# Kernel tuning notes

Measured on AMD Instinct MI355X. Metric: run time of the kernel, lower is better.

## Reference

```python
import jax, jax.numpy as jnp
import numpy as np

DIM = 512
NUM_HEADS = 8
HEAD_DIM = DIM // NUM_HEADS
B, S = 2, 2048


def setup_inputs() -> dict:
    key = jax.random.key(0)
    ks = jax.random.split(key, 16)
    scale = 1.0 / np.sqrt(DIM)
    inp = {
        "x": jax.random.normal(ks[0], (B, S, DIM), dtype=jnp.float32),
        "Qexpl": jax.random.normal(ks[1], (B, S, DIM), dtype=jnp.float32),
        "Kexpl": jax.random.normal(ks[2], (B, S, DIM), dtype=jnp.float32),
        "fl": jax.random.uniform(ks[3], (B,), dtype=jnp.float32),
        "fu": jax.random.uniform(ks[4], (B,), dtype=jnp.float32),
        "age": jax.random.uniform(ks[5], (B,), dtype=jnp.float32),
        "gender": jax.random.uniform(ks[6], (B,), dtype=jnp.float32),
        # Linear params: weight stored as [out, in] like torch; y = x @ W.T + b
        "Wq": jax.random.normal(ks[7], (DIM, DIM), dtype=jnp.float32) * scale,
        "bq": jnp.zeros((DIM,), dtype=jnp.float32),
        "Wk": jax.random.normal(ks[8], (DIM, DIM), dtype=jnp.float32) * scale,
        "bk": jnp.zeros((DIM,), dtype=jnp.float32),
        "Wv": jax.random.normal(ks[9], (DIM, DIM), dtype=jnp.float32) * scale,
        "bv": jnp.zeros((DIM,), dtype=jnp.float32),
        "Wo": jax.random.normal(ks[10], (DIM, DIM), dtype=jnp.float32) * scale,
        "bo": jnp.zeros((DIM,), dtype=jnp.float32),
    }
    return inp


def reference(x, Qexpl, Kexpl, fl, fu, age, gender, Wq, bq, Wk, bk, Wv, bv, Wo, bo):
    # drofe_fn is None -> Q/K projections used directly.
    Q = Qexpl @ Wq.T + bq            # [B, S, D]
    K = Kexpl @ Wk.T + bk            # [B, S, D]
    V = x @ Wv.T + bv                # [B, S, D]

    def split_heads(t):  # [B, S, D] -> [B, H, S, hd]
        return t.reshape(B, S, NUM_HEADS, HEAD_DIM).transpose(0, 2, 1, 3)

    Qh, Kh, Vh = split_heads(Q), split_heads(K), split_heads(V)
    scale = 1.0 / np.sqrt(HEAD_DIM).astype(np.float32)
    scores = jnp.einsum("bhqd,bhkd->bhqk", Qh, Kh) * scale  # [B, H, S, S]
    weights = jax.nn.softmax(scores, axis=-1)
    attn = jnp.einsum("bhqk,bhkd->bhqd", weights, Vh)        # [B, H, S, hd]
    attn = attn.transpose(0, 2, 1, 3).reshape(B, S, DIM)
    return attn @ Wo.T + bo
```

## Files before the change

kernel.cpp:

```cpp
#include <hip/hip_runtime.h>
#include <hip/hip_bf16.h>

typedef unsigned short ushort_t;
typedef __attribute__((ext_vector_type(8))) short bf16x8;
typedef __attribute__((ext_vector_type(4))) float f32x4;

__device__ __forceinline__ ushort_t f2bf(float f) {
    union { float f; unsigned u; } v; v.f = f;
    unsigned r = v.u + 0x7FFF + ((v.u >> 16) & 1);
    return (ushort_t)(r >> 16);
}
__device__ __forceinline__ bf16x8 ld8(const ushort_t* p) { return *(const bf16x8*)p; }

__device__ __forceinline__ unsigned cvt2(float x, float y) {
    __hip_bfloat162 h = __float22bfloat162_rn(make_float2(x, y));
    unsigned r; __builtin_memcpy(&r, &h, 4); return r;
}
__device__ __forceinline__ bf16x8 pack8(const float* p) {
    float4 a = *(const float4*)p;
    float4 b = *(const float4*)(p + 4);
    union { unsigned u[4]; bf16x8 v; } o;
    o.u[0] = cvt2(a.x, a.y); o.u[1] = cvt2(a.z, a.w);
    o.u[2] = cvt2(b.x, b.y); o.u[3] = cvt2(b.z, b.w);
    return o.v;
}

template <bool A_BF16, int OUT_MODE>
__device__ __forceinline__ void gemm_bt_tile(
    const void* __restrict__ Ap, const float* __restrict__ W,
    const float* __restrict__ bias, void* __restrict__ dstp,
    ushort_t* lA, ushort_t* lB, int m0, int n0)
{
    const ushort_t* Ab = (const ushort_t*)Ap;
    const float*    Af = (const float*)Ap;
    const int t = threadIdx.x;
    const int lane = t & 63;
    const int wave = t >> 6;
    const int wm = (wave & 1) * 64, wn = (wave >> 1) * 64;
    const int fr = lane & 15, quad = lane >> 4;

    f32x4 acc[4][4] = {};

    for (int k0 = 0; k0 < 512; k0 += 32) {
        bf16x8 va[2], vb[2];
#pragma unroll
        for (int i = 0; i < 2; ++i) {
            int s = i * 256 + t;
            int r = s >> 2, jp = s & 3;
            if (A_BF16)
                va[i] = ld8(Ab + (size_t)(m0 + r) * 512 + k0 + jp * 8);
            else
                va[i] = pack8(Af + (size_t)(m0 + r) * 512 + k0 + jp * 8);
            vb[i] = pack8(W + (size_t)(n0 + r) * 512 + k0 + jp * 8);
        }
        if (k0) __syncthreads();
#pragma unroll
        for (int i = 0; i < 2; ++i) {
            int s = i * 256 + t;
            int r = s >> 2, jp = s & 3;
            *(bf16x8*)(lA + r * 40 + jp * 8) = va[i];
            *(bf16x8*)(lB + r * 40 + jp * 8) = vb[i];
        }
        __syncthreads();

        bf16x8 af[4], bfrag[4];
#pragma unroll
        for (int mt = 0; mt < 4; ++mt)
            af[mt] = ld8(lA + (wm + mt * 16 + fr) * 40 + quad * 8);
#pragma unroll
        for (int nt = 0; nt < 4; ++nt)
            bfrag[nt] = ld8(lB + (wn + nt * 16 + fr) * 40 + quad * 8);
#pragma unroll
        for (int mt = 0; mt < 4; ++mt)
#pragma unroll
            for (int nt = 0; nt < 4; ++nt)
                acc[mt][nt] = __builtin_amdgcn_mfma_f32_16x16x32_bf16(
                    af[mt], bfrag[nt], acc[mt][nt], 0, 0, 0);
    }

#pragma unroll
    for (int nt = 0; nt < 4; ++nt) {
        int n = n0 + wn + nt * 16 + fr;
        float bb = bias[n];
#pragma unroll
        for (int mt = 0; mt < 4; ++mt) {
            int mb = m0 + wm + mt * 16 + quad * 4;
            if (OUT_MODE == 0) {
#pragma unroll
                for (int r = 0; r < 4; ++r)
                    ((ushort_t*)dstp)[(size_t)(mb + r) * 512 + n] = f2bf(acc[mt][nt][r] + bb);
            } else if (OUT_MODE == 1) {
#pragma unroll
                for (int r = 0; r < 4; ++r)
                    ((float*)dstp)[(size_t)(mb + r) * 512 + n] = acc[mt][nt][r] + bb;
            } else {
                int h = n >> 6, d = n & 63;
                int bidx = mb >> 11, s = mb & 2047;
                ushort4 pk;
                pk.x = f2bf(acc[mt][nt][0] + bb);
                pk.y = f2bf(acc[mt][nt][1] + bb);
                pk.z = f2bf(acc[mt][nt][2] + bb);
                pk.w = f2bf(acc[mt][nt][3] + bb);
                *(ushort4*)((ushort_t*)dstp + ((size_t)((bidx * 8 + h) * 64 + d)) * 2048 + s) = pk;
            }
        }
    }
}

__global__ __launch_bounds__(256, 2)
void proj_qkv_kernel(const float* __restrict__ Qe, const float* __restrict__ Ke,
                     const float* __restrict__ x,
                     const float* __restrict__ Wq, const float* __restrict__ bq,
                     const float* __restrict__ Wk, const float* __restrict__ bk,
                     const float* __restrict__ Wv, const float* __restrict__ bv,
                     ushort_t* __restrict__ Qo, ushort_t* __restrict__ Ko,
                     ushort_t* __restrict__ Vt)
{
    __shared__ ushort_t lA[128 * 40];
    __shared__ ushort_t lB[128 * 40];
    const int z = blockIdx.z;
    const float* A = (z == 0) ? Qe : (z == 1) ? Ke : x;
    const float* W = (z == 0) ? Wq : (z == 1) ? Wk : Wv;
    const float* bias = (z == 0) ? bq : (z == 1) ? bk : bv;
    ushort_t* dst = (z == 0) ? Qo : (z == 1) ? Ko : Vt;
    if (z == 2)
        gemm_bt_tile<false, 2>(A, W, bias, dst, lA, lB, blockIdx.y * 128, blockIdx.x * 128);
    else
        gemm_bt_tile<false, 0>(A, W, bias, dst, lA, lB, blockIdx.y * 128, blockIdx.x * 128);
}

__global__ __launch_bounds__(256, 2)
void gemm_o_kernel(const ushort_t* __restrict__ A, const float* __restrict__ W,
                   const float* __restrict__ bias, float* __restrict__ dst)
{
    __shared__ ushort_t lA[128 * 40];
    __shared__ ushort_t lB[128 * 40];
    gemm_bt_tile<true, 1>(A, W, bias, dst, lA, lB, blockIdx.y * 128, blockIdx.x * 128);
}

__global__ __launch_bounds__(256, 2)
void attn_kernel(const ushort_t* __restrict__ Q, const ushort_t* __restrict__ K,
                 const ushort_t* __restrict__ Vt, ushort_t* __restrict__ O)
{
    __shared__ ushort_t lQ[64 * 72];
    __shared__ ushort_t lK[128 * 72];
    __shared__ ushort_t lVt[64 * 136];
    __shared__ ushort_t lP[64 * 136];

    const int b = blockIdx.z, h = blockIdx.y;
    const int q0 = blockIdx.x * 64;
    const int t = threadIdx.x;
    const int lane = t & 63, wave = t >> 6;
    const int wq = wave * 16;
    const int fr = lane & 15, quad = lane >> 4;

#pragma unroll
    for (int i = 0; i < 2; ++i) {
        int s = i * 256 + t;
        int r = s >> 3, jp = s & 7;
        *(bf16x8*)(lQ + r * 72 + jp * 8) =
            ld8(Q + (size_t)(b * 2048 + q0 + r) * 512 + h * 64 + jp * 8);
    }

    const float C1 = 0.125f * 1.44269504088896340736f;
    const float FM = 12.0f;

    f32x4 oacc[4] = {};
    float lpart[4] = {};

    for (int kv = 0; kv < 2048; kv += 128) {
        bf16x8 vk[4], vv[4];
#pragma unroll
        for (int i = 0; i < 4; ++i) {
            int s = i * 256 + t;
            int r = s >> 3, jp = s & 7;
            vk[i] = ld8(K + (size_t)(b * 2048 + kv + r) * 512 + h * 64 + jp * 8);
            int r2 = s >> 4, jp2 = s & 15;
            vv[i] = ld8(Vt + (size_t)((b * 8 + h) * 64 + r2) * 2048 + kv + jp2 * 8);
        }
        __syncthreads();
#pragma unroll
        for (int i = 0; i < 4; ++i) {
            int s = i * 256 + t;
            int r = s >> 3, jp = s & 7;
            *(bf16x8*)(lK + r * 72 + jp * 8) = vk[i];
            int r2 = s >> 4, jp2 = s & 15;
            *(bf16x8*)(lVt + r2 * 136 + jp2 * 8) = vv[i];
        }
        __syncthreads();

        f32x4 sc[8] = {};
#pragma unroll
        for (int ks = 0; ks < 2; ++ks) {
            bf16x8 aq = ld8(lQ + (wq + fr) * 72 + (ks * 4 + quad) * 8);
#pragma unroll
            for (int nt = 0; nt < 8; ++nt) {
                bf16x8 kb = ld8(lK + (nt * 16 + fr) * 72 + (ks * 4 + quad) * 8);
                sc[nt] = __builtin_amdgcn_mfma_f32_16x16x32_bf16(aq, kb, sc[nt], 0, 0, 0);
            }
        }

#pragma unroll
        for (int r = 0; r < 4; ++r) {
            int row = wq + quad * 4 + r;
            float acc = 0.f;
#pragma unroll
            for (int nt = 0; nt < 8; ++nt) {
                float p = exp2f(sc[nt][r] * C1 - FM);
                acc += p;
                lP[row * 136 + nt * 16 + fr] = f2bf(p);
            }
            lpart[r] += acc;
        }

#pragma unroll
        for (int ks = 0; ks < 4; ++ks) {
            bf16x8 ap = ld8(lP + (wq + fr) * 136 + ks * 32 + quad * 8);
#pragma unroll
            for (int nt = 0; nt < 4; ++nt) {
                bf16x8 vb = ld8(lVt + (nt * 16 + fr) * 136 + ks * 32 + quad * 8);
                oacc[nt] = __builtin_amdgcn_mfma_f32_16x16x32_bf16(ap, vb, oacc[nt], 0, 0, 0);
            }
        }
    }

#pragma unroll
    for (int r = 0; r < 4; ++r) {
        float rs = lpart[r];
#pragma unroll
        for (int o = 1; o < 16; o <<= 1)
            rs += __shfl_xor(rs, o, 64);
        float inv = 1.f / rs;
        int q = q0 + wq + quad * 4 + r;
#pragma unroll
        for (int nt = 0; nt < 4; ++nt) {
            int d = nt * 16 + fr;
            O[(size_t)(b * 2048 + q) * 512 + h * 64 + d] = f2bf(oacc[nt][r] * inv);
        }
    }
}

extern "C" void kernel_launch(void* const* d_in, const int* in_sizes, int n_in,
                              void* d_out, int out_size, void* d_ws, size_t ws_size,
                              hipStream_t stream) {
    const float* x   = (const float*)d_in[0];
    const float* Qe  = (const float*)d_in[1];
    const float* Ke  = (const float*)d_in[2];
    const float* Wq  = (const float*)d_in[7];
    const float* bq  = (const float*)d_in[8];
    const float* Wk  = (const float*)d_in[9];
    const float* bk  = (const float*)d_in[10];
    const float* Wv  = (const float*)d_in[11];
    const float* bv  = (const float*)d_in[12];
    const float* Wo  = (const float*)d_in[13];
    const float* bo  = (const float*)d_in[14];

    const size_t NTOK = 2 * 2048;
    ushort_t* Qws = (ushort_t*)d_ws;
    ushort_t* Kws = Qws + NTOK * 512;
    ushort_t* Vt  = Kws + NTOK * 512;
    ushort_t* Ows = Vt  + NTOK * 512;

    proj_qkv_kernel<<<dim3(4, 32, 3), 256, 0, stream>>>(Qe, Ke, x, Wq, bq, Wk, bk, Wv, bv,
                                                        Qws, Kws, Vt);
    attn_kernel<<<dim3(32, 8, 2), 256, 0, stream>>>(Qws, Kws, Vt, Ows);
    gemm_o_kernel<<<dim3(4, 32, 1), 256, 0, stream>>>(Ows, Wo, bo, (float*)d_out);
}
```

Before: 182.8 us.

## Pre-convert inputs to bf16 and stage GEMM tiles via global_load_lds

Adds a conversion kernel that turns the fp32 activations and weights into bf16 up front. The GEMMs then load tiles straight into LDS with global_load_lds instead of converting in registers. The fused QKV launch is split into three separate GEMM launches, and the output projection uses 64-row tiles to put more blocks on the device. The attention softmax now packs P with paired bf16 conversion. The cost is an extra kernel launch plus a full fp32 read and bf16 write of the inputs, and the unpadded 32-wide LDS rows may cause bank conflicts.

```diff
diff --git a/kernel.cpp b/kernel.cpp
--- a/kernel.cpp
+++ b/kernel.cpp
@@ -16,60 +16,65 @@
     __hip_bfloat162 h = __float22bfloat162_rn(make_float2(x, y));
     unsigned r; __builtin_memcpy(&r, &h, 4); return r;
 }
-__device__ __forceinline__ bf16x8 pack8(const float* p) {
-    float4 a = *(const float4*)p;
-    float4 b = *(const float4*)(p + 4);
-    union { unsigned u[4]; bf16x8 v; } o;
-    o.u[0] = cvt2(a.x, a.y); o.u[1] = cvt2(a.z, a.w);
-    o.u[2] = cvt2(b.x, b.y); o.u[3] = cvt2(b.z, b.w);
-    return o.v;
-}
-
-template <bool A_BF16, int OUT_MODE>
-__device__ __forceinline__ void gemm_bt_tile(
-    const void* __restrict__ Ap, const float* __restrict__ W,
-    const float* __restrict__ bias, void* __restrict__ dstp,
-    ushort_t* lA, ushort_t* lB, int m0, int n0)
+
+__device__ __forceinline__ void gll16(const ushort_t* g, ushort_t* l) {
+    __builtin_amdgcn_global_load_lds(
+        (const __attribute__((address_space(1))) unsigned int*)g,
+        (__attribute__((address_space(3))) unsigned int*)l, 16, 0, 0);
+}
+
+struct CvtArgs { const float* src[7]; ushort_t* dst[7]; int n[7]; };
+
+__global__ __launch_bounds__(256)
+void cvt_kernel(CvtArgs a) {
+    const int seg = blockIdx.y;
+    const float* s = a.src[seg];
+    ushort_t* d = a.dst[seg];
+    const int n = a.n[seg];
+    for (int i = (blockIdx.x * 256 + threadIdx.x) * 8; i < n; i += gridDim.x * 256 * 8) {
+        float4 x = *(const float4*)(s + i);
+        float4 y = *(const float4*)(s + i + 4);
+        union { unsigned u[4]; ushort4 v[2]; } o;
+        o.u[0] = cvt2(x.x, x.y); o.u[1] = cvt2(x.z, x.w);
+        o.u[2] = cvt2(y.x, y.y); o.u[3] = cvt2(y.z, y.w);
+        *(ushort4*)(d + i) = o.v[0];
+        *(ushort4*)(d + i + 4) = o.v[1];
+    }
+}
+
+template <int OUT_MODE>
+__global__ __launch_bounds__(256, 2)
+void gemm128_kernel(const ushort_t* __restrict__ A, const ushort_t* __restrict__ W,
+                    const float* __restrict__ bias, void* __restrict__ dstp)
 {
-    const ushort_t* Ab = (const ushort_t*)Ap;
-    const float*    Af = (const float*)Ap;
+    __shared__ ushort_t lA[128 * 32];
+    __shared__ ushort_t lB[128 * 32];
+    const int m0 = blockIdx.y * 128, n0 = blockIdx.x * 128;
     const int t = threadIdx.x;
-    const int lane = t & 63;
-    const int wave = t >> 6;
+    const int lane = t & 63, wave = t >> 6;
     const int wm = (wave & 1) * 64, wn = (wave >> 1) * 64;
     const int fr = lane & 15, quad = lane >> 4;
 
     f32x4 acc[4][4] = {};
 
     for (int k0 = 0; k0 < 512; k0 += 32) {
-        bf16x8 va[2], vb[2];
+        if (k0) __syncthreads();
 #pragma unroll
         for (int i = 0; i < 2; ++i) {
             int s = i * 256 + t;
             int r = s >> 2, jp = s & 3;
-            if (A_BF16)
-                va[i] = ld8(Ab + (size_t)(m0 + r) * 512 + k0 + jp * 8);
-            else
-                va[i] = pack8(Af + (size_t)(m0 + r) * 512 + k0 + jp * 8);
-            vb[i] = pack8(W + (size_t)(n0 + r) * 512 + k0 + jp * 8);
-        }
-        if (k0) __syncthreads();
-#pragma unroll
-        for (int i = 0; i < 2; ++i) {
-            int s = i * 256 + t;
-            int r = s >> 2, jp = s & 3;
-            *(bf16x8*)(lA + r * 40 + jp * 8) = va[i];
-            *(bf16x8*)(lB + r * 40 + jp * 8) = vb[i];
+            gll16(A + (size_t)(m0 + r) * 512 + k0 + jp * 8, lA + s * 8);
+            gll16(W + (size_t)(n0 + r) * 512 + k0 + jp * 8, lB + s * 8);
         }
         __syncthreads();
 
         bf16x8 af[4], bfrag[4];
 #pragma unroll
         for (int mt = 0; mt < 4; ++mt)
-            af[mt] = ld8(lA + (wm + mt * 16 + fr) * 40 + quad * 8);
+            af[mt] = ld8(lA + (wm + mt * 16 + fr) * 32 + quad * 8);
 #pragma unroll
         for (int nt = 0; nt < 4; ++nt)
-            bfrag[nt] = ld8(lB + (wn + nt * 16 + fr) * 40 + quad * 8);
+            bfrag[nt] = ld8(lB + (wn + nt * 16 + fr) * 32 + quad * 8);
 #pragma unroll
         for (int mt = 0; mt < 4; ++mt)
 #pragma unroll
@@ -96,46 +101,70 @@
             } else {
                 int h = n >> 6, d = n & 63;
                 int bidx = mb >> 11, s = mb & 2047;
-                ushort4 pk;
-                pk.x = f2bf(acc[mt][nt][0] + bb);
-                pk.y = f2bf(acc[mt][nt][1] + bb);
-                pk.z = f2bf(acc[mt][nt][2] + bb);
-                pk.w = f2bf(acc[mt][nt][3] + bb);
-                *(ushort4*)((ushort_t*)dstp + ((size_t)((bidx * 8 + h) * 64 + d)) * 2048 + s) = pk;
+                union { unsigned u[2]; ushort4 v; } pk;
+                pk.u[0] = cvt2(acc[mt][nt][0] + bb, acc[mt][nt][1] + bb);
+                pk.u[1] = cvt2(acc[mt][nt][2] + bb, acc[mt][nt][3] + bb);
+                *(ushort4*)((ushort_t*)dstp + ((size_t)((bidx * 8 + h) * 64 + d)) * 2048 + s) = pk.v;
             }
         }
     }
 }
 
 __global__ __launch_bounds__(256, 2)
-void proj_qkv_kernel(const float* __restrict__ Qe, const float* __restrict__ Ke,
-                     const float* __restrict__ x,
-                     const float* __restrict__ Wq, const float* __restrict__ bq,
-                     const float* __restrict__ Wk, const float* __restrict__ bk,
-                     const float* __restrict__ Wv, const float* __restrict__ bv,
-                     ushort_t* __restrict__ Qo, ushort_t* __restrict__ Ko,
-                     ushort_t* __restrict__ Vt)
-{
-    __shared__ ushort_t lA[128 * 40];
-    __shared__ ushort_t lB[128 * 40];
-    const int z = blockIdx.z;
-    const float* A = (z == 0) ? Qe : (z == 1) ? Ke : x;
-    const float* W = (z == 0) ? Wq : (z == 1) ? Wk : Wv;
-    const float* bias = (z == 0) ? bq : (z == 1) ? bk : bv;
-    ushort_t* dst = (z == 0) ? Qo : (z == 1) ? Ko : Vt;
-    if (z == 2)
-        gemm_bt_tile<false, 2>(A, W, bias, dst, lA, lB, blockIdx.y * 128, blockIdx.x * 128);
-    else
-        gemm_bt_tile<false, 0>(A, W, bias, dst, lA, lB, blockIdx.y * 128, blockIdx.x * 128);
-}
-
-__global__ __launch_bounds__(256, 2)
-void gemm_o_kernel(const ushort_t* __restrict__ A, const float* __restrict__ W,
+void gemm64_kernel(const ushort_t* __restrict__ A, const ushort_t* __restrict__ W,
                    const float* __restrict__ bias, float* __restrict__ dst)
 {
-    __shared__ ushort_t lA[128 * 40];
-    __shared__ ushort_t lB[128 * 40];
-    gemm_bt_tile<true, 1>(A, W, bias, dst, lA, lB, blockIdx.y * 128, blockIdx.x * 128);
+    __shared__ ushort_t lA[64 * 32];
+    __shared__ ushort_t lB[128 * 32];
+    const int m0 = blockIdx.y * 64, n0 = blockIdx.x * 128;
+    const int t = threadIdx.x;
+    const int lane = t & 63, wave = t >> 6;
+    const int wm = (wave & 1) * 32, wn = (wave >> 1) * 64;
+    const int fr = lane & 15, quad = lane >> 4;
+
+    f32x4 acc[2][4] = {};
+
+    for (int k0 = 0; k0 < 512; k0 += 32) {
+        if (k0) __syncthreads();
+        {
+            int r = t >> 2, jp = t & 3;
+            gll16(A + (size_t)(m0 + r) * 512 + k0 + jp * 8, lA + t * 8);
+        }
+#pragma unroll
+        for (int i = 0; i < 2; ++i) {
+            int s = i * 256 + t;
+            int r = s >> 2, jp = s & 3;
+            gll16(W + (size_t)(n0 + r) * 512 + k0 + jp * 8, lB + s * 8);
+        }
+        __syncthreads();
+
+        bf16x8 af[2], bfrag[4];
+#pragma unroll
+        for (int mt = 0; mt < 2; ++mt)
+            af[mt] = ld8(lA + (wm + mt * 16 + fr) * 32 + quad * 8);
+#pragma unroll
+        for (int nt = 0; nt < 4; ++nt)
+            bfrag[nt] = ld8(lB + (wn + nt * 16 + fr) * 32 + quad * 8);
+#pragma unroll
+        for (int mt = 0; mt < 2; ++mt)
+#pragma unroll
+            for (int nt = 0; nt < 4; ++nt)
+                acc[mt][nt] = __builtin_amdgcn_mfma_f32_16x16x32_bf16(
+                    af[mt], bfrag[nt], acc[mt][nt], 0, 0, 0);
+    }
+
+#pragma unroll
+    for (int nt = 0; nt < 4; ++nt) {
+        int n = n0 + wn + nt * 16 + fr;
+        float bb = bias[n];
+#pragma unroll
+        for (int mt = 0; mt < 2; ++mt) {
+            int mb = m0 + wm + mt * 16 + quad * 4;
+#pragma unroll
+            for (int r = 0; r < 4; ++r)
+                dst[(size_t)(mb + r) * 512 + n] = acc[mt][nt][r] + bb;
+        }
+    }
 }
 
 __global__ __launch_bounds__(256, 2)
@@ -203,14 +232,20 @@
 #pragma unroll
         for (int r = 0; r < 4; ++r) {
             int row = wq + quad * 4 + r;
+            float pv[8];
             float acc = 0.f;
 #pragma unroll
             for (int nt = 0; nt < 8; ++nt) {
-                float p = exp2f(sc[nt][r] * C1 - FM);
-                acc += p;
-                lP[row * 136 + nt * 16 + fr] = f2bf(p);
+                pv[nt] = exp2f(sc[nt][r] * C1 - FM);
+                acc += pv[nt];
             }
             lpart[r] += acc;
+            union { unsigned u[4]; ushort_t us[8]; } pu;
+            pu.u[0] = cvt2(pv[0], pv[1]); pu.u[1] = cvt2(pv[2], pv[3]);
+            pu.u[2] = cvt2(pv[4], pv[5]); pu.u[3] = cvt2(pv[6], pv[7]);
+#pragma unroll
+            for (int nt = 0; nt < 8; ++nt)
+                lP[row * 136 + nt * 16 + fr] = pu.us[nt];
         }
 
 #pragma unroll
@@ -256,13 +291,35 @@
     const float* bo  = (const float*)d_in[14];
 
     const size_t NTOK = 2 * 2048;
-    ushort_t* Qws = (ushort_t*)d_ws;
-    ushort_t* Kws = Qws + NTOK * 512;
-    ushort_t* Vt  = Kws + NTOK * 512;
-    ushort_t* Ows = Vt  + NTOK * 512;
-
-    proj_qkv_kernel<<<dim3(4, 32, 3), 256, 0, stream>>>(Qe, Ke, x, Wq, bq, Wk, bk, Wv, bv,
-                                                        Qws, Kws, Vt);
+    const size_t ACT = NTOK * 512;
+    const size_t WSZ = 512 * 512;
+
+    ushort_t* p = (ushort_t*)d_ws;
+    ushort_t* xb  = p; p += ACT;
+    ushort_t* Qeb = p; p += ACT;
+    ushort_t* Keb = p; p += ACT;
+    ushort_t* Wqb = p; p += WSZ;
+    ushort_t* Wkb = p; p += WSZ;
+    ushort_t* Wvb = p; p += WSZ;
+    ushort_t* Wob = p; p += WSZ;
+    ushort_t* Qws = p; p += ACT;
+    ushort_t* Kws = p; p += ACT;
+    ushort_t* Vt  = p; p += ACT;
+    ushort_t* Ows = p; p += ACT;
+
+    CvtArgs ca;
+    ca.src[0] = x;  ca.dst[0] = xb;  ca.n[0] = (int)ACT;
+    ca.src[1] = Qe; ca.dst[1] = Qeb; ca.n[1] = (int)ACT;
+    ca.src[2] = Ke; ca.dst[2] = Keb; ca.n[2] = (int)ACT;
+    ca.src[3] = Wq; ca.dst[3] = Wqb; ca.n[3] = (int)WSZ;
+    ca.src[4] = Wk; ca.dst[4] = Wkb; ca.n[4] = (int)WSZ;
+    ca.src[5] = Wv; ca.dst[5] = Wvb; ca.n[5] = (int)WSZ;
+    ca.src[6] = Wo; ca.dst[6] = Wob; ca.n[6] = (int)WSZ;
+    cvt_kernel<<<dim3(512, 7), 256, 0, stream>>>(ca);
+
+    gemm128_kernel<0><<<dim3(4, 32), 256, 0, stream>>>(Qeb, Wqb, bq, Qws);
+    gemm128_kernel<0><<<dim3(4, 32), 256, 0, stream>>>(Keb, Wkb, bk, Kws);
+    gemm128_kernel<2><<<dim3(4, 32), 256, 0, stream>>>(xb,  Wvb, bv, Vt);
     attn_kernel<<<dim3(32, 8, 2), 256, 0, stream>>>(Qws, Kws, Vt, Ows);
-    gemm_o_kernel<<<dim3(4, 32, 1), 256, 0, stream>>>(Ows, Wo, bo, (float*)d_out);
-}
+    gemm64_kernel<<<dim3(4, 64), 256, 0, stream>>>(Ows, Wob, bo, (float*)d_out);
+}
```

Result: slower. 192.7 us (+5.4%).
